# Kernel tuning notes

Measured on AMD Instinct MI355X. Metric: run time of the kernel, lower is better.

## Reference

```python
import jax, jax.numpy as jnp
import numpy as np

N, D, K = 65536, 512, 4096


def setup_inputs() -> dict:
    key = jax.random.key(0)
    kx, kc = jax.random.split(key)
    x = jax.random.normal(kx, (N, D), dtype=jnp.float32)
    center = jax.random.normal(kc, (K, D), dtype=jnp.float32)
    return {"x": x, "center": center}


def squared_euclidean(x, center):
    x_sq = jnp.sum(x * x, axis=1, keepdims=True)        # [N,1]
    c_sq = jnp.sum(center * center, axis=1)             # [K]
    cross = x @ center.T                                # [N,K] GEMM
    return x_sq - 2.0 * cross + c_sq[None, :]


def reference(x, center):
    # KMeans.forward: dis_func(input, center).argmin(1)
    dist = squared_euclidean(x, center)                 # [N,K]
    return jnp.argmin(dist, axis=1)                     # [N] int32
```

## Files before the change

kernel.cpp:

```cpp
#include <hip/hip_runtime.h>

#define N_ROWS 65536
#define DIM    512
#define K_CENT 4096
#define TILE_M 128
#define TILE_N 128
#define BK     64
#define KSTEPS (DIM / BK)
#define NKT    (K_CENT / TILE_N)
#define NSTEP  (NKT * KSTEPS)
#define THREADS 512
#define MARGIN 22.0f
#define CAND_CAP 1536
#define COMPACT_TRIG 1024
#define SCALE1 0x7F7F7F7F

typedef float  floatx4  __attribute__((ext_vector_type(4)));
typedef float  floatx16 __attribute__((ext_vector_type(16)));
typedef int    intx2    __attribute__((ext_vector_type(2)));
typedef int    intx4    __attribute__((ext_vector_type(4)));
typedef int    intx8    __attribute__((ext_vector_type(8)));

__device__ __forceinline__ unsigned mapF(float f) {
  unsigned u = __float_as_uint(f);
  return (u & 0x80000000u) ? ~u : (u | 0x80000000u);
}
__device__ __forceinline__ float unmapF(unsigned m) {
  unsigned u = (m & 0x80000000u) ? (m ^ 0x80000000u) : ~m;
  return __uint_as_float(u);
}

__device__ __forceinline__ void gload_lds16(const void* g, void* l) {
  __builtin_amdgcn_global_load_lds(
      (const __attribute__((address_space(1))) void*)g,
      (__attribute__((address_space(3))) void*)l, 16, 0, 0);
}

__device__ __forceinline__ int pk4(float a, float b, float c, float d) {
  int r = __builtin_amdgcn_cvt_pk_fp8_f32(a, b, 0, false);
  r = __builtin_amdgcn_cvt_pk_fp8_f32(c, d, r, true);
  return r;
}

#define FENCE_BAR() do { asm volatile("s_waitcnt lgkmcnt(0)" ::: "memory"); \
                         __builtin_amdgcn_s_barrier();                       \
                         __builtin_amdgcn_sched_barrier(0); } while (0)

__global__ void prep_convert(const float* __restrict__ x, const float* __restrict__ c,
                             unsigned char* __restrict__ xq, unsigned char* __restrict__ cq,
                             float* __restrict__ csqg) {
  const size_t nx = (size_t)N_ROWS * DIM;
  size_t i = ((size_t)blockIdx.x * blockDim.x + threadIdx.x) * 16;
  if (i < nx) {
    floatx4 a0 = *(const floatx4*)(x + i);
    floatx4 a1 = *(const floatx4*)(x + i + 4);
    floatx4 a2 = *(const floatx4*)(x + i + 8);
    floatx4 a3 = *(const floatx4*)(x + i + 12);
    intx4 q = { pk4(a0[0],a0[1],a0[2],a0[3]), pk4(a1[0],a1[1],a1[2],a1[3]),
                pk4(a2[0],a2[1],a2[2],a2[3]), pk4(a3[0],a3[1],a3[2],a3[3]) };
    *(intx4*)(xq + i) = q;
  } else if (i < nx + (size_t)K_CENT * DIM) {
    size_t off = i - nx;
    floatx4 a0 = *(const floatx4*)(c + off);
    floatx4 a1 = *(const floatx4*)(c + off + 4);
    floatx4 a2 = *(const floatx4*)(c + off + 8);
    floatx4 a3 = *(const floatx4*)(c + off + 12);
    intx4 q = { pk4(a0[0],a0[1],a0[2],a0[3]), pk4(a1[0],a1[1],a1[2],a1[3]),
                pk4(a2[0],a2[1],a2[2],a2[3]), pk4(a3[0],a3[1],a3[2],a3[3]) };
    *(intx4*)(cq + off) = q;
    float s = 0.f;
#pragma unroll
    for (int e = 0; e < 4; ++e)
      s += a0[e]*a0[e] + a1[e]*a1[e] + a2[e]*a2[e] + a3[e]*a3[e];
#pragma unroll
    for (int o = 1; o < 32; o <<= 1) s += __shfl_xor(s, o, 64);
    if ((threadIdx.x & 31) == 0) csqg[off >> 9] = s;
  }
}

__global__ __launch_bounds__(THREADS, 2)
void kmeans_argmin_pipe(const float* __restrict__ x, const float* __restrict__ cent,
                        const unsigned char* __restrict__ xq, const unsigned char* __restrict__ cq,
                        const float* __restrict__ csqg, int* __restrict__ out) {
  extern __shared__ __align__(16) unsigned char dynLds[];
  unsigned char* ldsA = dynLds;
  unsigned char* ldsB = dynLds + 3 * 8192;
  __shared__ float csqL[K_CENT];
  __shared__ unsigned sminU[TILE_M];
  __shared__ unsigned long long best[TILE_M];
  __shared__ unsigned candKey[CAND_CAP];
  __shared__ float candS[CAND_CAP];
  __shared__ int candCount;

  const int t = threadIdx.x;
  const int lane = t & 63;
  const int wave = t >> 6;
  const int wm = wave >> 1;
  const int wn = wave & 1;
  const int l31 = lane & 31;
  const int half = lane >> 5;
  const int rowBlock = blockIdx.x * TILE_M;

  if (t < TILE_M) { sminU[t] = 0xFFFFFFFFu; best[t] = ~0ull; }
  if (t == 0) candCount = 0;
  for (int i = t; i < K_CENT; i += THREADS) csqL[i] = csqg[i];

  const int rS = (t >> 2) & 31;
  const int rowS = (t >> 7) * 32 + rS;
  const int offS = (((t & 3) ^ ((rS >> 1) & 3)) << 4);
  const int qk = half * 2;
  const int fragSlotBase = 4 * l31 + (qk ^ ((l31 >> 1) & 3));

  const size_t aRowOff = (size_t)(rowBlock + rowS) * DIM + offS;

  asm volatile("s_waitcnt vmcnt(0)" ::: "memory");
  gload_lds16(xq + aRowOff + 0,  ldsA + wave * 1024);
  gload_lds16(cq + (size_t)rowS * DIM + 0 + offS,  ldsB + wave * 1024);
  gload_lds16(xq + aRowOff + 64, ldsA + 8192 + wave * 1024);
  gload_lds16(cq + (size_t)rowS * DIM + 64 + offS, ldsB + 8192 + wave * 1024);
  FENCE_BAR();

  floatx16 acc[2];
#pragma unroll
  for (int fn = 0; fn < 2; ++fn)
#pragma unroll
    for (int e = 0; e < 16; ++e) acc[fn][e] = 0.f;

  int bi = 0;
  for (int j = 0; j < NSTEP; ++j) {
    const int kt = j >> 3, ks = j & 7;
    if (j + 2 < NSTEP) {
      const int j2 = j + 2;
      const int kt2 = j2 >> 3, ks2 = j2 & 7;
      int b2 = bi + 2; if (b2 >= 3) b2 -= 3;
      gload_lds16(xq + aRowOff + (ks2 << 6), ldsA + (b2 << 13) + wave * 1024);
      gload_lds16(cq + (size_t)((kt2 << 7) + rowS) * DIM + (ks2 << 6) + offS,
                  ldsB + (b2 << 13) + wave * 1024);
      asm volatile("s_waitcnt vmcnt(4)" ::: "memory");
    } else if (j + 2 == NSTEP) {
      asm volatile("s_waitcnt vmcnt(2)" ::: "memory");
    } else {
      asm volatile("s_waitcnt vmcnt(0)" ::: "memory");
    }
    __builtin_amdgcn_s_barrier();
    __builtin_amdgcn_sched_barrier(0);

    const unsigned char* A = ldsA + (bi << 13);
    const unsigned char* B = ldsB + (bi << 13);
    intx8 aF, bF[2];
    {
      int s0 = wm * 128 + fragSlotBase;
      intx4 lo = *(const intx4*)(A + s0 * 16);
      intx4 hi = *(const intx4*)(A + (s0 ^ 1) * 16);
      aF = (intx8){lo[0], lo[1], lo[2], lo[3], hi[0], hi[1], hi[2], hi[3]};
    }
#pragma unroll
    for (int fn = 0; fn < 2; ++fn) {
      int s0 = (wn * 2 + fn) * 128 + fragSlotBase;
      intx4 lo = *(const intx4*)(B + s0 * 16);
      intx4 hi = *(const intx4*)(B + (s0 ^ 1) * 16);
      bF[fn] = (intx8){lo[0], lo[1], lo[2], lo[3], hi[0], hi[1], hi[2], hi[3]};
    }
    asm volatile("s_waitcnt lgkmcnt(0)" ::: "memory");
    __builtin_amdgcn_sched_barrier(0);
#pragma unroll
    for (int fn = 0; fn < 2; ++fn)
      acc[fn] = __builtin_amdgcn_mfma_scale_f32_32x32x64_f8f6f4(
          aF, bF[fn], acc[fn], 0, 0, 0, SCALE1, 0, SCALE1);

    if (ks == KSTEPS - 1) {
      const int ktBase = kt << 7;
      float cs[2];
#pragma unroll
      for (int fn = 0; fn < 2; ++fn)
        cs[fn] = csqL[ktBase + wn * 64 + fn * 32 + l31];

#pragma unroll
      for (int r = 0; r < 16; ++r) {
        float v = fminf(cs[0] - 2.f * acc[0][r], cs[1] - 2.f * acc[1][r]);
        v = fminf(v, __shfl_xor(v, 1, 64));
        v = fminf(v, __shfl_xor(v, 2, 64));
        v = fminf(v, __shfl_xor(v, 4, 64));
        v = fminf(v, __shfl_xor(v, 8, 64));
        v = fminf(v, __shfl_xor(v, 16, 64));
        if (l31 == 0) {
          int srow = wm * 32 + (r & 3) + 8 * (r >> 2) + 4 * half;
          atomicMin(&sminU[srow], mapF(v));
        }
      }
      FENCE_BAR();

#pragma unroll
      for (int r = 0; r < 16; ++r) {
        int srow = wm * 32 + (r & 3) + 8 * (r >> 2) + 4 * half;
        float thr = unmapF(sminU[srow]) + MARGIN;
#pragma unroll
        for (int fn = 0; fn < 2; ++fn) {
          float s = cs[fn] - 2.f * acc[fn][r];
          if (s <= thr) {
            int k = ktBase + wn * 64 + fn * 32 + l31;
            int idx = atomicAdd(&candCount, 1);
            if (idx < CAND_CAP) {
              candKey[idx] = ((unsigned)k << 7) | (unsigned)srow;
              candS[idx] = s;
            }
          }
        }
      }
      FENCE_BAR();

      if (candCount > COMPACT_TRIG) {
        int cc = candCount; if (cc > CAND_CAP) cc = CAND_CAP;
        unsigned myK[4]; float myS[4]; int myN = 0;
        for (int i = t; i < cc; i += THREADS) {
          int rl = candKey[i] & 127;
          if (candS[i] <= unmapF(sminU[rl]) + MARGIN && myN < 4) {
            myK[myN] = candKey[i]; myS[myN] = candS[i]; ++myN;
          }
        }
        FENCE_BAR();
        if (t == 0) candCount = 0;
        FENCE_BAR();
        int base = atomicAdd(&candCount, myN);
        for (int jj = 0; jj < myN; ++jj) { candKey[base + jj] = myK[jj]; candS[base + jj] = myS[jj]; }
        FENCE_BAR();
      }

#pragma unroll
      for (int fn = 0; fn < 2; ++fn)
#pragma unroll
        for (int e = 0; e < 16; ++e) acc[fn][e] = 0.f;
    } else {
      __builtin_amdgcn_s_barrier();
      __builtin_amdgcn_sched_barrier(0);
    }
    ++bi; if (bi == 3) bi = 0;
  }

  __syncthreads();

  int cnt = candCount; if (cnt > CAND_CAP) cnt = CAND_CAP;
  const int g = t >> 4;
  const int sl = t & 15;
  for (int ci = g; ci < cnt; ci += 32) {
    unsigned cd = candKey[ci];
    int rl = cd & 127;
    if (candS[ci] > unmapF(sminU[rl]) + MARGIN) continue;
    int k = cd >> 7;
    const float* xr = x + (size_t)(rowBlock + rl) * DIM;
    const float* cr = cent + (size_t)k * DIM;
    double d = 0.0;
#pragma unroll
    for (int jj = 0; jj < DIM / 64; ++jj) {
      floatx4 xv = *(const floatx4*)(xr + jj * 64 + sl * 4);
      floatx4 cv = *(const floatx4*)(cr + jj * 64 + sl * 4);
#pragma unroll
      for (int e = 0; e < 4; ++e) {
        double df = (double)xv[e] - (double)cv[e];
        d += df * df;
      }
    }
#pragma unroll
    for (int off = 1; off < 16; off <<= 1) d += __shfl_xor(d, off, 64);
    if (sl == 0) {
      unsigned long long key =
          ((unsigned long long)__double_as_longlong(d) & ~0xFFFull) | (unsigned long long)k;
      atomicMin(&best[rl], key);
    }
  }
  __syncthreads();
  if (t < TILE_M) out[rowBlock + t] = (int)(best[t] & 0xFFFull);
}

__global__ __launch_bounds__(THREADS, 4)
void kmeans_argmin_fb(const float* __restrict__ x, const float* __restrict__ cent,
                      int* __restrict__ out) {
  __shared__ unsigned char ldsA[TILE_M * BK];
  __shared__ unsigned char ldsB[TILE_N * BK];
  __shared__ float csq4[TILE_N][4];
  __shared__ unsigned sminU[TILE_M];
  __shared__ unsigned long long best[TILE_M];
  __shared__ unsigned candKey[CAND_CAP];
  __shared__ float candS[CAND_CAP];
  __shared__ int candCount;

  const int t = threadIdx.x;
  const int lane = t & 63;
  const int wave = t >> 6;
  const int wm = wave >> 1;
  const int wn = wave & 1;
  const int l31 = lane & 31;
  const int half = lane >> 5;
  const int rowBlock = blockIdx.x * TILE_M;

  if (t < TILE_M) { sminU[t] = 0xFFFFFFFFu; best[t] = ~0ull; }
  if (t == 0) candCount = 0;

  const int rS = (t >> 2) & 31;
  const int rowS = (t >> 7) * 32 + rS;
  const int offS = (((t & 3) ^ ((rS >> 1) & 3)) << 4);
  const int qk = half * 2;
  const int fragSlotBase = 4 * l31 + (qk ^ ((l31 >> 1) & 3));

  for (int kt = 0; kt < NKT; ++kt) {
    const int ktBase = kt * TILE_N;
    ((float*)csq4)[t] = 0.f;
    floatx16 acc[2];
#pragma unroll
    for (int fn = 0; fn < 2; ++fn)
#pragma unroll
      for (int e = 0; e < 16; ++e) acc[fn][e] = 0.f;

    for (int ks = 0; ks < KSTEPS; ++ks) {
      const int kd = ks * BK;
      {
        const float* gA = x + (size_t)(rowBlock + rowS) * DIM + kd + offS;
        floatx4 f0 = *(const floatx4*)gA, f1 = *(const floatx4*)(gA + 4);
        floatx4 f2 = *(const floatx4*)(gA + 8), f3 = *(const floatx4*)(gA + 12);
        intx4 q = { pk4(f0[0],f0[1],f0[2],f0[3]), pk4(f1[0],f1[1],f1[2],f1[3]),
                    pk4(f2[0],f2[1],f2[2],f2[3]), pk4(f3[0],f3[1],f3[2],f3[3]) };
        *(intx4*)(ldsA + (size_t)t * 16) = q;
      }
      {
        const float* gB = cent + (size_t)(ktBase + rowS) * DIM + kd + offS;
        floatx4 f0 = *(const floatx4*)gB, f1 = *(const floatx4*)(gB + 4);
        floatx4 f2 = *(const floatx4*)(gB + 8), f3 = *(const floatx4*)(gB + 12);
        intx4 q = { pk4(f0[0],f0[1],f0[2],f0[3]), pk4(f1[0],f1[1],f1[2],f1[3]),
                    pk4(f2[0],f2[1],f2[2],f2[3]), pk4(f3[0],f3[1],f3[2],f3[3]) };
        *(intx4*)(ldsB + (size_t)t * 16) = q;
        float s = 0.f;
#pragma unroll
        for (int e = 0; e < 4; ++e)
          s += f0[e]*f0[e] + f1[e]*f1[e] + f2[e]*f2[e] + f3[e]*f3[e];
        csq4[rowS][t & 3] += s;
      }
      __syncthreads();

      intx8 aF, bF[2];
      {
        int s0 = wm * 128 + fragSlotBase;
        intx4 lo = *(const intx4*)(ldsA + s0 * 16);
        intx4 hi = *(const intx4*)(ldsA + (s0 ^ 1) * 16);
        aF = (intx8){lo[0], lo[1], lo[2], lo[3], hi[0], hi[1], hi[2], hi[3]};
      }
#pragma unroll
      for (int fn = 0; fn < 2; ++fn) {
        int s0 = (wn * 2 + fn) * 128 + fragSlotBase;
        intx4 lo = *(const intx4*)(ldsB + s0 * 16);
        intx4 hi = *(const intx4*)(ldsB + (s0 ^ 1) * 16);
        bF[fn] = (intx8){lo[0], lo[1], lo[2], lo[3], hi[0], hi[1], hi[2], hi[3]};
      }
#pragma unroll
      for (int fn = 0; fn < 2; ++fn)
        acc[fn] = __builtin_amdgcn_mfma_scale_f32_32x32x64_f8f6f4(
            aF, bF[fn], acc[fn], 0, 0, 0, SCALE1, 0, SCALE1);
      __syncthreads();
    }

    float cs[2];
#pragma unroll
    for (int fn = 0; fn < 2; ++fn) {
      int cl = wn * 64 + fn * 32 + l31;
      cs[fn] = csq4[cl][0] + csq4[cl][1] + csq4[cl][2] + csq4[cl][3];
    }

#pragma unroll
    for (int r = 0; r < 16; ++r) {
      float v = fminf(cs[0] - 2.f * acc[0][r], cs[1] - 2.f * acc[1][r]);
      v = fminf(v, __shfl_xor(v, 1, 64));
      v = fminf(v, __shfl_xor(v, 2, 64));
      v = fminf(v, __shfl_xor(v, 4, 64));
      v = fminf(v, __shfl_xor(v, 8, 64));
      v = fminf(v, __shfl_xor(v, 16, 64));
      if (l31 == 0) {
        int srow = wm * 32 + (r & 3) + 8 * (r >> 2) + 4 * half;
        atomicMin(&sminU[srow], mapF(v));
      }
    }
    __syncthreads();

#pragma unroll
    for (int r = 0; r < 16; ++r) {
      int srow = wm * 32 + (r & 3) + 8 * (r >> 2) + 4 * half;
      float thr = unmapF(sminU[srow]) + MARGIN;
#pragma unroll
      for (int fn = 0; fn < 2; ++fn) {
        float s = cs[fn] - 2.f * acc[fn][r];
        if (s <= thr) {
          int k = ktBase + wn * 64 + fn * 32 + l31;
          int idx = atomicAdd(&candCount, 1);
          if (idx < CAND_CAP) {
            candKey[idx] = ((unsigned)k << 7) | (unsigned)srow;
            candS[idx] = s;
          }
        }
      }
    }
    __syncthreads();

    if (candCount > COMPACT_TRIG) {
      int cc = candCount; if (cc > CAND_CAP) cc = CAND_CAP;
      unsigned myK[4]; float myS[4]; int myN = 0;
      for (int i = t; i < cc; i += THREADS) {
        int rl = candKey[i] & 127;
        if (candS[i] <= unmapF(sminU[rl]) + MARGIN && myN < 4) {
          myK[myN] = candKey[i]; myS[myN] = candS[i]; ++myN;
        }
      }
      __syncthreads();
      if (t == 0) candCount = 0;
      __syncthreads();
      int base = atomicAdd(&candCount, myN);
      for (int j = 0; j < myN; ++j) { candKey[base + j] = myK[j]; candS[base + j] = myS[j]; }
      __syncthreads();
    }
  }

  int cnt = candCount; if (cnt > CAND_CAP) cnt = CAND_CAP;
  const int g = t >> 4;
  const int sl = t & 15;
  for (int ci = g; ci < cnt; ci += 32) {
    unsigned cd = candKey[ci];
    int rl = cd & 127;
    if (candS[ci] > unmapF(sminU[rl]) + MARGIN) continue;
    int k = cd >> 7;
    const float* xr = x + (size_t)(rowBlock + rl) * DIM;
    const float* cr = cent + (size_t)k * DIM;
    double d = 0.0;
#pragma unroll
    for (int j = 0; j < DIM / 64; ++j) {
      floatx4 xv = *(const floatx4*)(xr + j * 64 + sl * 4);
      floatx4 cv = *(const floatx4*)(cr + j * 64 + sl * 4);
#pragma unroll
      for (int e = 0; e < 4; ++e) {
        double df = (double)xv[e] - (double)cv[e];
        d += df * df;
      }
    }
#pragma unroll
    for (int off = 1; off < 16; off <<= 1) d += __shfl_xor(d, off, 64);
    if (sl == 0) {
      unsigned long long key =
          ((unsigned long long)__double_as_longlong(d) & ~0xFFFull) | (unsigned long long)k;
      atomicMin(&best[rl], key);
    }
  }
  __syncthreads();
  if (t < TILE_M) out[rowBlock + t] = (int)(best[t] & 0xFFFull);
}

extern "C" void kernel_launch(void* const* d_in, const int* in_sizes, int n_in,
                              void* d_out, int out_size, void* d_ws, size_t ws_size,
                              hipStream_t stream) {
  const float* x = (const float*)d_in[0];
  const float* cent = (const float*)d_in[1];
  int* out = (int*)d_out;
  const size_t nXq = (size_t)N_ROWS * DIM;
  const size_t nCq = (size_t)K_CENT * DIM;
  const size_t nCsq = (size_t)K_CENT * sizeof(float);
  const int grid = N_ROWS / TILE_M;

  if (ws_size >= nXq + nCq + nCsq) {
    unsigned char* xq = (unsigned char*)d_ws;
    unsigned char* cq = xq + nXq;
    float* csqg = (float*)(cq + nCq);
    const size_t total16 = ((size_t)N_ROWS + K_CENT) * DIM / 16;
    prep_convert<<<(unsigned)((total16 + 255) / 256), 256, 0, stream>>>(x, cent, xq, cq, csqg);
    kmeans_argmin_pipe<<<grid, THREADS, 6 * 8192, stream>>>(x, cent, xq, cq, csqg, out);
  } else {
    kmeans_argmin_fb<<<grid, THREADS, 0, stream>>>(x, cent, out);
  }
}
```

Baseline: 623.6 us.

## Keep FP8 x fragments in registers, stream only centroids through LDS

The x rows are no longer pre-converted to FP8 in a separate pass. Each wave now converts its own 32 rows directly into register-resident MFMA fragments covering the full 512-dim depth, and only centroid tiles stream through a 4-buffer LDS ring. The MFMA operand order is swapped so each lane holds one row, which lets the per-row min and candidate thresholding use one cross-half shuffle instead of a five-step reduction, and occupancy is raised to 4 blocks. The aim is to cut the x quantisation traffic and the per-step LDS A loads and barriers, at the cost of many extra VGPRs for the x fragments and possible spilling under the tighter launch bound.

```diff
diff --git a/kernel.cpp b/kernel.cpp
--- a/kernel.cpp
+++ b/kernel.cpp
@@ -8,7 +8,6 @@
 #define BK     64
 #define KSTEPS (DIM / BK)
 #define NKT    (K_CENT / TILE_N)
-#define NSTEP  (NKT * KSTEPS)
 #define THREADS 512
 #define MARGIN 22.0f
 #define CAND_CAP 1536
@@ -46,45 +45,31 @@
                          __builtin_amdgcn_s_barrier();                       \
                          __builtin_amdgcn_sched_barrier(0); } while (0)
 
-__global__ void prep_convert(const float* __restrict__ x, const float* __restrict__ c,
-                             unsigned char* __restrict__ xq, unsigned char* __restrict__ cq,
-                             float* __restrict__ csqg) {
-  const size_t nx = (size_t)N_ROWS * DIM;
+__global__ void prep_convert(const float* __restrict__ c,
+                             unsigned char* __restrict__ cq, float* __restrict__ csqg) {
   size_t i = ((size_t)blockIdx.x * blockDim.x + threadIdx.x) * 16;
-  if (i < nx) {
-    floatx4 a0 = *(const floatx4*)(x + i);
-    floatx4 a1 = *(const floatx4*)(x + i + 4);
-    floatx4 a2 = *(const floatx4*)(x + i + 8);
-    floatx4 a3 = *(const floatx4*)(x + i + 12);
-    intx4 q = { pk4(a0[0],a0[1],a0[2],a0[3]), pk4(a1[0],a1[1],a1[2],a1[3]),
-                pk4(a2[0],a2[1],a2[2],a2[3]), pk4(a3[0],a3[1],a3[2],a3[3]) };
-    *(intx4*)(xq + i) = q;
-  } else if (i < nx + (size_t)K_CENT * DIM) {
-    size_t off = i - nx;
-    floatx4 a0 = *(const floatx4*)(c + off);
-    floatx4 a1 = *(const floatx4*)(c + off + 4);
-    floatx4 a2 = *(const floatx4*)(c + off + 8);
-    floatx4 a3 = *(const floatx4*)(c + off + 12);
-    intx4 q = { pk4(a0[0],a0[1],a0[2],a0[3]), pk4(a1[0],a1[1],a1[2],a1[3]),
-                pk4(a2[0],a2[1],a2[2],a2[3]), pk4(a3[0],a3[1],a3[2],a3[3]) };
-    *(intx4*)(cq + off) = q;
-    float s = 0.f;
-#pragma unroll
-    for (int e = 0; e < 4; ++e)
-      s += a0[e]*a0[e] + a1[e]*a1[e] + a2[e]*a2[e] + a3[e]*a3[e];
-#pragma unroll
-    for (int o = 1; o < 32; o <<= 1) s += __shfl_xor(s, o, 64);
-    if ((threadIdx.x & 31) == 0) csqg[off >> 9] = s;
-  }
-}
-
-__global__ __launch_bounds__(THREADS, 2)
+  if (i >= (size_t)K_CENT * DIM) return;
+  floatx4 a0 = *(const floatx4*)(c + i);
+  floatx4 a1 = *(const floatx4*)(c + i + 4);
+  floatx4 a2 = *(const floatx4*)(c + i + 8);
+  floatx4 a3 = *(const floatx4*)(c + i + 12);
+  intx4 q = { pk4(a0[0],a0[1],a0[2],a0[3]), pk4(a1[0],a1[1],a1[2],a1[3]),
+              pk4(a2[0],a2[1],a2[2],a2[3]), pk4(a3[0],a3[1],a3[2],a3[3]) };
+  *(intx4*)(cq + i) = q;
+  float s = 0.f;
+#pragma unroll
+  for (int e = 0; e < 4; ++e)
+    s += a0[e]*a0[e] + a1[e]*a1[e] + a2[e]*a2[e] + a3[e]*a3[e];
+#pragma unroll
+  for (int o = 1; o < 32; o <<= 1) s += __shfl_xor(s, o, 64);
+  if ((threadIdx.x & 31) == 0) csqg[i >> 9] = s;
+}
+
+__global__ __launch_bounds__(THREADS, 4)
 void kmeans_argmin_pipe(const float* __restrict__ x, const float* __restrict__ cent,
-                        const unsigned char* __restrict__ xq, const unsigned char* __restrict__ cq,
+                        const unsigned char* __restrict__ cq,
                         const float* __restrict__ csqg, int* __restrict__ out) {
   extern __shared__ __align__(16) unsigned char dynLds[];
-  unsigned char* ldsA = dynLds;
-  unsigned char* ldsB = dynLds + 3 * 8192;
   __shared__ float csqL[K_CENT];
   __shared__ unsigned sminU[TILE_M];
   __shared__ unsigned long long best[TILE_M];
@@ -100,141 +85,132 @@
   const int l31 = lane & 31;
   const int half = lane >> 5;
   const int rowBlock = blockIdx.x * TILE_M;
+  const int srow = wm * 32 + l31;
 
   if (t < TILE_M) { sminU[t] = 0xFFFFFFFFu; best[t] = ~0ull; }
   if (t == 0) candCount = 0;
-  for (int i = t; i < K_CENT; i += THREADS) csqL[i] = csqg[i];
+#pragma unroll
+  for (int i = 0; i < K_CENT / THREADS; ++i) {
+    int idx = t + i * THREADS;
+    csqL[idx] = csqg[idx];
+  }
 
   const int rS = (t >> 2) & 31;
   const int rowS = (t >> 7) * 32 + rS;
   const int offS = (((t & 3) ^ ((rS >> 1) & 3)) << 4);
+  unsigned bOff = (unsigned)(rowS * DIM + offS);
+
   const int qk = half * 2;
   const int fragSlotBase = 4 * l31 + (qk ^ ((l31 >> 1) & 3));
-
-  const size_t aRowOff = (size_t)(rowBlock + rowS) * DIM + offS;
+  const unsigned char* pB0  = dynLds + (((wn * 2 + 0) * 128 + fragSlotBase) * 16);
+  const unsigned char* pB0x = dynLds + ((((wn * 2 + 0) * 128 + fragSlotBase) ^ 1) * 16);
+  const unsigned char* pB1  = dynLds + (((wn * 2 + 1) * 128 + fragSlotBase) * 16);
+  const unsigned char* pB1x = dynLds + ((((wn * 2 + 1) * 128 + fragSlotBase) ^ 1) * 16);
+
+  intx8 xf[KSTEPS];
+  {
+    const float* xr = x + (size_t)(rowBlock + srow) * DIM + half * 32;
+#pragma unroll
+    for (int ks = 0; ks < KSTEPS; ++ks) {
+      int q[8];
+#pragma unroll
+      for (int j = 0; j < 8; ++j) {
+        floatx4 f = *(const floatx4*)(xr + ks * 64 + j * 4);
+        q[j] = pk4(f[0], f[1], f[2], f[3]);
+      }
+      xf[ks] = (intx8){q[0], q[1], q[2], q[3], q[4], q[5], q[6], q[7]};
+    }
+  }
 
   asm volatile("s_waitcnt vmcnt(0)" ::: "memory");
-  gload_lds16(xq + aRowOff + 0,  ldsA + wave * 1024);
-  gload_lds16(cq + (size_t)rowS * DIM + 0 + offS,  ldsB + wave * 1024);
-  gload_lds16(xq + aRowOff + 64, ldsA + 8192 + wave * 1024);
-  gload_lds16(cq + (size_t)rowS * DIM + 64 + offS, ldsB + 8192 + wave * 1024);
+  gload_lds16(cq + bOff, dynLds + 0 * 8192 + wave * 1024); bOff += 64;
+  gload_lds16(cq + bOff, dynLds + 1 * 8192 + wave * 1024); bOff += 64;
   FENCE_BAR();
 
-  floatx16 acc[2];
-#pragma unroll
-  for (int fn = 0; fn < 2; ++fn)
-#pragma unroll
-    for (int e = 0; e < 16; ++e) acc[fn][e] = 0.f;
-
-  int bi = 0;
-  for (int j = 0; j < NSTEP; ++j) {
-    const int kt = j >> 3, ks = j & 7;
-    if (j + 2 < NSTEP) {
-      const int j2 = j + 2;
-      const int kt2 = j2 >> 3, ks2 = j2 & 7;
-      int b2 = bi + 2; if (b2 >= 3) b2 -= 3;
-      gload_lds16(xq + aRowOff + (ks2 << 6), ldsA + (b2 << 13) + wave * 1024);
-      gload_lds16(cq + (size_t)((kt2 << 7) + rowS) * DIM + (ks2 << 6) + offS,
-                  ldsB + (b2 << 13) + wave * 1024);
-      asm volatile("s_waitcnt vmcnt(4)" ::: "memory");
-    } else if (j + 2 == NSTEP) {
+  for (int kt = 0; kt < NKT; ++kt) {
+    floatx16 acc[2];
+#pragma unroll
+    for (int fn = 0; fn < 2; ++fn)
+#pragma unroll
+      for (int e = 0; e < 16; ++e) acc[fn][e] = 0.f;
+
+#pragma unroll
+    for (int p = 0; p < KSTEPS; ++p) {
+      gload_lds16(cq + bOff, dynLds + (((p + 2) & 3) << 13) + wave * 1024);
+      bOff += (p == 5) ? (65536 - 7 * 64) : 64;
       asm volatile("s_waitcnt vmcnt(2)" ::: "memory");
-    } else {
-      asm volatile("s_waitcnt vmcnt(0)" ::: "memory");
-    }
-    __builtin_amdgcn_s_barrier();
-    __builtin_amdgcn_sched_barrier(0);
-
-    const unsigned char* A = ldsA + (bi << 13);
-    const unsigned char* B = ldsB + (bi << 13);
-    intx8 aF, bF[2];
+      __builtin_amdgcn_s_barrier();
+      __builtin_amdgcn_sched_barrier(0);
+
+      const int bo = (p & 3) << 13;
+      intx4 lo0 = *(const intx4*)(pB0  + bo);
+      intx4 hi0 = *(const intx4*)(pB0x + bo);
+      intx4 lo1 = *(const intx4*)(pB1  + bo);
+      intx4 hi1 = *(const intx4*)(pB1x + bo);
+      asm volatile("s_waitcnt lgkmcnt(0)" ::: "memory");
+      __builtin_amdgcn_sched_barrier(0);
+      intx8 b0 = (intx8){lo0[0], lo0[1], lo0[2], lo0[3], hi0[0], hi0[1], hi0[2], hi0[3]};
+      intx8 b1 = (intx8){lo1[0], lo1[1], lo1[2], lo1[3], hi1[0], hi1[1], hi1[2], hi1[3]};
+      acc[0] = __builtin_amdgcn_mfma_scale_f32_32x32x64_f8f6f4(
+          b0, xf[p], acc[0], 0, 0, 0, SCALE1, 0, SCALE1);
+      acc[1] = __builtin_amdgcn_mfma_scale_f32_32x32x64_f8f6f4(
+          b1, xf[p], acc[1], 0, 0, 0, SCALE1, 0, SCALE1);
+    }
+
+    const int ktBase = kt << 7;
+    float mn = 3.4e38f;
+#pragma unroll
+    for (int fn = 0; fn < 2; ++fn)
+#pragma unroll
+      for (int g = 0; g < 4; ++g) {
+        floatx4 cs4 = *(const floatx4*)&csqL[ktBase + (wn * 2 + fn) * 32 + 8 * g + 4 * half];
+#pragma unroll
+        for (int e = 0; e < 4; ++e)
+          mn = fminf(mn, cs4[e] - 2.f * acc[fn][4 * g + e]);
+      }
+    mn = fminf(mn, __shfl_xor(mn, 32, 64));
+    if (half == 0) atomicMin(&sminU[srow], mapF(mn));
+    FENCE_BAR();
+
     {
-      int s0 = wm * 128 + fragSlotBase;
-      intx4 lo = *(const intx4*)(A + s0 * 16);
-      intx4 hi = *(const intx4*)(A + (s0 ^ 1) * 16);
-      aF = (intx8){lo[0], lo[1], lo[2], lo[3], hi[0], hi[1], hi[2], hi[3]};
-    }
-#pragma unroll
-    for (int fn = 0; fn < 2; ++fn) {
-      int s0 = (wn * 2 + fn) * 128 + fragSlotBase;
-      intx4 lo = *(const intx4*)(B + s0 * 16);
-      intx4 hi = *(const intx4*)(B + (s0 ^ 1) * 16);
-      bF[fn] = (intx8){lo[0], lo[1], lo[2], lo[3], hi[0], hi[1], hi[2], hi[3]};
-    }
-    asm volatile("s_waitcnt lgkmcnt(0)" ::: "memory");
-    __builtin_amdgcn_sched_barrier(0);
-#pragma unroll
-    for (int fn = 0; fn < 2; ++fn)
-      acc[fn] = __builtin_amdgcn_mfma_scale_f32_32x32x64_f8f6f4(
-          aF, bF[fn], acc[fn], 0, 0, 0, SCALE1, 0, SCALE1);
-
-    if (ks == KSTEPS - 1) {
-      const int ktBase = kt << 7;
-      float cs[2];
+      float thr = unmapF(sminU[srow]) + MARGIN;
 #pragma unroll
       for (int fn = 0; fn < 2; ++fn)
-        cs[fn] = csqL[ktBase + wn * 64 + fn * 32 + l31];
-
-#pragma unroll
-      for (int r = 0; r < 16; ++r) {
-        float v = fminf(cs[0] - 2.f * acc[0][r], cs[1] - 2.f * acc[1][r]);
-        v = fminf(v, __shfl_xor(v, 1, 64));
-        v = fminf(v, __shfl_xor(v, 2, 64));
-        v = fminf(v, __shfl_xor(v, 4, 64));
-        v = fminf(v, __shfl_xor(v, 8, 64));
-        v = fminf(v, __shfl_xor(v, 16, 64));
-        if (l31 == 0) {
-          int srow = wm * 32 + (r & 3) + 8 * (r >> 2) + 4 * half;
-          atomicMin(&sminU[srow], mapF(v));
-        }
-      }
-      FENCE_BAR();
-
-#pragma unroll
-      for (int r = 0; r < 16; ++r) {
-        int srow = wm * 32 + (r & 3) + 8 * (r >> 2) + 4 * half;
-        float thr = unmapF(sminU[srow]) + MARGIN;
-#pragma unroll
-        for (int fn = 0; fn < 2; ++fn) {
-          float s = cs[fn] - 2.f * acc[fn][r];
-          if (s <= thr) {
-            int k = ktBase + wn * 64 + fn * 32 + l31;
-            int idx = atomicAdd(&candCount, 1);
-            if (idx < CAND_CAP) {
-              candKey[idx] = ((unsigned)k << 7) | (unsigned)srow;
-              candS[idx] = s;
+#pragma unroll
+        for (int g = 0; g < 4; ++g) {
+          floatx4 cs4 = *(const floatx4*)&csqL[ktBase + (wn * 2 + fn) * 32 + 8 * g + 4 * half];
+#pragma unroll
+          for (int e = 0; e < 4; ++e) {
+            float s = cs4[e] - 2.f * acc[fn][4 * g + e];
+            if (s <= thr) {
+              int k = ktBase + (wn * 2 + fn) * 32 + 8 * g + 4 * half + e;
+              int idx = atomicAdd(&candCount, 1);
+              if (idx < CAND_CAP) {
+                candKey[idx] = ((unsigned)k << 7) | (unsigned)srow;
+                candS[idx] = s;
+              }
             }
           }
         }
+    }
+    FENCE_BAR();
+
+    if (candCount > COMPACT_TRIG) {
+      int cc = candCount; if (cc > CAND_CAP) cc = CAND_CAP;
+      unsigned myK[4]; float myS[4]; int myN = 0;
+      for (int i = t; i < cc; i += THREADS) {
+        int rl = candKey[i] & 127;
+        if (candS[i] <= unmapF(sminU[rl]) + MARGIN && myN < 4) {
+          myK[myN] = candKey[i]; myS[myN] = candS[i]; ++myN;
+        }
       }
       FENCE_BAR();
-
-      if (candCount > COMPACT_TRIG) {
-        int cc = candCount; if (cc > CAND_CAP) cc = CAND_CAP;
-        unsigned myK[4]; float myS[4]; int myN = 0;
-        for (int i = t; i < cc; i += THREADS) {
-          int rl = candKey[i] & 127;
-          if (candS[i] <= unmapF(sminU[rl]) + MARGIN && myN < 4) {
-            myK[myN] = candKey[i]; myS[myN] = candS[i]; ++myN;
-          }
-        }
-        FENCE_BAR();
-        if (t == 0) candCount = 0;
-        FENCE_BAR();
-        int base = atomicAdd(&candCount, myN);
-        for (int jj = 0; jj < myN; ++jj) { candKey[base + jj] = myK[jj]; candS[base + jj] = myS[jj]; }
-        FENCE_BAR();
-      }
-
-#pragma unroll
-      for (int fn = 0; fn < 2; ++fn)
-#pragma unroll
-        for (int e = 0; e < 16; ++e) acc[fn][e] = 0.f;
-    } else {
-      __builtin_amdgcn_s_barrier();
-      __builtin_amdgcn_sched_barrier(0);
-    }
-    ++bi; if (bi == 3) bi = 0;
+      if (t == 0) candCount = 0;
+      FENCE_BAR();
+      int base = atomicAdd(&candCount, myN);
+      for (int jj = 0; jj < myN; ++jj) { candKey[base + jj] = myK[jj]; candS[base + jj] = myS[jj]; }
+      FENCE_BAR();
+    }
   }
 
   __syncthreads();
@@ -461,12 +437,11 @@
   const int grid = N_ROWS / TILE_M;
 
   if (ws_size >= nXq + nCq + nCsq) {
-    unsigned char* xq = (unsigned char*)d_ws;
-    unsigned char* cq = xq + nXq;
+    unsigned char* cq = (unsigned char*)d_ws;
     float* csqg = (float*)(cq + nCq);
-    const size_t total16 = ((size_t)N_ROWS + K_CENT) * DIM / 16;
-    prep_convert<<<(unsigned)((total16 + 255) / 256), 256, 0, stream>>>(x, cent, xq, cq, csqg);
-    kmeans_argmin_pipe<<<grid, THREADS, 6 * 8192, stream>>>(x, cent, xq, cq, csqg, out);
+    const size_t total16 = nCq / 16;
+    prep_convert<<<(unsigned)((total16 + 255) / 256), 256, 0, stream>>>(cent, cq, csqg);
+    kmeans_argmin_pipe<<<grid, THREADS, 4 * 8192, stream>>>(x, cent, cq, csqg, out);
   } else {
     kmeans_argmin_fb<<<grid, THREADS, 0, stream>>>(x, cent, out);
   }
```

After: 601.9 us. 1.04x faster.
